# Kernel tuning notes

Hardware: AMD Instinct MI355X
Metric: run time of the kernel (lower is better)

## Reference

```python
import jax, jax.numpy as jnp
import numpy as np

N, F_IN, H, C1, CH, NCLS, E = 10000, 512, 8, 30, 64, 64, 160000


def gat_conv(x, src, dst, W, a_src, a_dst, b):
    # x: [N, Fin]; W: [Fin, H*C]; a_src/a_dst: [H, C]; b: [H*C]
    n, = (x.shape[0],)
    C = a_src.shape[1]
    h = (x @ W).reshape(n, H, C)                        # [N,H,C]
    asrc = jnp.einsum('nhc,hc->nh', h, a_src)           # [N,H]
    adst = jnp.einsum('nhc,hc->nh', h, a_dst)           # [N,H]
    alpha = jax.nn.leaky_relu(asrc[src] + adst[dst], 0.2)  # [E,H]
    # segment softmax over incoming edges of each destination node
    m = jax.ops.segment_max(alpha, dst, num_segments=n)
    m = jax.lax.stop_gradient(jnp.where(jnp.isfinite(m), m, 0.0))
    e = jnp.exp(alpha - m[dst])
    s = jax.ops.segment_sum(e, dst, num_segments=n)
    w = e / (s[dst] + 1e-16)                            # [E,H]
    out = jax.ops.segment_sum(w[:, :, None] * h[src], dst, num_segments=n)
    return out.reshape(n, H * C) + b


def setup_inputs() -> dict:
    key = jax.random.key(0)
    ks = jax.random.split(key, 12)
    x = jax.random.normal(ks[0], (N, F_IN), dtype=jnp.float32)
    edge_index = jax.random.randint(ks[1], (2, E), 0, N, dtype=jnp.int64)
    sc = lambda fin: 1.0 / np.sqrt(fin)
    return {
        'x': x,
        'edge_index': edge_index,
        'W1': jax.random.normal(ks[2], (F_IN, H * C1), jnp.float32) * sc(F_IN),
        'a1_src': jax.random.normal(ks[3], (H, C1), jnp.float32) * sc(C1),
        'a1_dst': jax.random.normal(ks[4], (H, C1), jnp.float32) * sc(C1),
        'b1': jnp.zeros((H * C1,), jnp.float32),
        'W2': jax.random.normal(ks[5], (H * C1, H * CH), jnp.float32) * sc(H * C1),
        'a2_src': jax.random.normal(ks[6], (H, CH), jnp.float32) * sc(CH),
        'a2_dst': jax.random.normal(ks[7], (H, CH), jnp.float32) * sc(CH),
        'b2': jnp.zeros((H * CH,), jnp.float32),
        'Wlin': jax.random.normal(ks[8], (H * CH, NCLS), jnp.float32) * sc(H * CH),
        'blin': jnp.zeros((NCLS,), jnp.float32),
    }


def reference(x, edge_index, W1, a1_src, a1_dst, b1, W2, a2_src, a2_dst, b2, Wlin, blin):
    n = x.shape[0]
    loops = jnp.arange(n, dtype=edge_index.dtype)
    src = jnp.concatenate([edge_index[0], loops])
    dst = jnp.concatenate([edge_index[1], loops])
    # dropout is identity in eval mode
    h1 = jax.nn.elu(gat_conv(x, src, dst, W1, a1_src, a1_dst, b1))
    h = gat_conv(h1, src, dst, W2, a2_src, a2_dst, b2)
    out = h @ Wlin + blin
    return (out, h)
```

## Files before the change

kernel.cpp:

```cpp
#include <hip/hip_runtime.h>
#include <type_traits>

typedef unsigned short ushort_t;
typedef float v4f __attribute__((ext_vector_type(4)));
typedef short v8s __attribute__((ext_vector_type(8)));
typedef unsigned short u16x8 __attribute__((ext_vector_type(8)));
typedef unsigned short u16x4v __attribute__((ext_vector_type(4)));

#define NN    10000
#define NP    10048
#define EE    160000
#define FIN   512
#define NH    8
#define C1    30
#define HC1   240
#define HC1P  256
#define C2    64
#define HC2   512
#define NCLS  64

#define TS1 (HC1P * FIN)
#define TS2 (HC2 * HC1P)
#define TS3 (NCLS * HC2)
#define XS  (NN * FIN / 4)

#define GLOBAL_AS __attribute__((address_space(1)))
#define LDS_AS    __attribute__((address_space(3)))

__device__ __forceinline__ void async_cp16(const void* g, void* l) {
    __builtin_amdgcn_global_load_lds((const GLOBAL_AS unsigned int*)g,
                                     (LDS_AS unsigned int*)l, 16, 0, 0);
}


__global__ __launch_bounds__(1024) void scan_kernel(const int* __restrict__ counts,
                                                    int* __restrict__ row_start,
                                                    int* __restrict__ cursor, int n) {
    __shared__ int sums[1024];
    int t = threadIdx.x;
    const int chunk = (n + 1023) / 1024;
    int beg = t * chunk;
    int end = min(beg + chunk, n);
    int s = 0;
    for (int i = beg; i < end; ++i) s += counts[i];
    sums[t] = s;
    __syncthreads();
    for (int off = 1; off < 1024; off <<= 1) {
        int v = (t >= off) ? sums[t - off] : 0;
        __syncthreads();
        sums[t] += v;
        __syncthreads();
    }
    int run = (t == 0) ? 0 : sums[t - 1];
    for (int i = beg; i < end; ++i) {
        row_start[i] = run;
        cursor[i] = run;
        run += counts[i];
    }
    if (t == 1023) row_start[n] = sums[1023];
}

__global__ __launch_bounds__(256) void scatter_kernel(const int* __restrict__ src,
                                                      const int* __restrict__ dst,
                                                      int* __restrict__ cursor,
                                                      int* __restrict__ edge_src, int E) {
    int e = blockIdx.x * blockDim.x + threadIdx.x;
    if (e < E) {
        int d = dst[e];
        int pos = atomicAdd(&cursor[d], 1);
        edge_src[pos] = src[e];
    }
}


__device__ __forceinline__ void split1(float v, ushort_t& h, ushort_t& l) {
    unsigned u = __float_as_uint(v);
    unsigned rh = u + 0x7FFFu + ((u >> 16) & 1u);
    h = (ushort_t)(rh >> 16);
    float hf = __uint_as_float((unsigned)h << 16);
    float rem = v - hf;
    unsigned u2 = __float_as_uint(rem);
    unsigned rl = u2 + 0x7FFFu + ((u2 >> 16) & 1u);
    l = (ushort_t)(rl >> 16);
}

__device__ __forceinline__ ushort_t f2bf(float v) {
    unsigned u = __float_as_uint(v);
    return (ushort_t)((u + 0x7FFFu + ((u >> 16) & 1u)) >> 16);
}

__device__ __forceinline__ float bf2f(ushort_t u) {
    return __uint_as_float((unsigned)u << 16);
}


__global__ __launch_bounds__(256) void prep_kernel(
    const float* __restrict__ x,
    const float* __restrict__ W1, const float* __restrict__ W2,
    const float* __restrict__ Wl,
    const float* __restrict__ a1s, const float* __restrict__ a1d,
    const int* __restrict__ dst,
    ushort_t* __restrict__ xh, ushort_t* __restrict__ xl,
    ushort_t* __restrict__ t1h, ushort_t* __restrict__ t1l,
    ushort_t* __restrict__ t2h, ushort_t* __restrict__ t2l,
    ushort_t* __restrict__ t3h, ushort_t* __restrict__ t3l,
    float* __restrict__ a1sP, float* __restrict__ a1dP,
    int* __restrict__ counts) {
    int idx = blockIdx.x * 256 + threadIdx.x;
    if (idx < XS) {
        int i = idx << 2;
        float4 v = *(const float4*)(x + i);
        ushort_t h, l;
        u16x4v hh, ll;
        split1(v.x, h, l); hh[0] = h; ll[0] = l;
        split1(v.y, h, l); hh[1] = h; ll[1] = l;
        split1(v.z, h, l); hh[2] = h; ll[2] = l;
        split1(v.w, h, l); hh[3] = h; ll[3] = l;
        *(u16x4v*)(xh + i) = hh;
        *(u16x4v*)(xl + i) = ll;
        return;
    }
    idx -= XS;
    if (idx < TS1) {
        int n = idx >> 9, k = idx & 511;
        int cc = n & 31;
        float v = (cc < 30) ? W1[(size_t)k * HC1 + ((n >> 5) * 30 + cc)] : 0.f;
        ushort_t h, l;
        split1(v, h, l);
        t1h[idx] = h;
        t1l[idx] = l;
    } else if (idx < TS1 + TS2) {
        int lo = idx - TS1;
        int n = lo >> 8, k = lo & 255;
        int cc = k & 31;
        float v = (cc < 30) ? W2[(size_t)((k >> 5) * 30 + cc) * HC2 + n] : 0.f;
        ushort_t h, l;
        split1(v, h, l);
        t2h[lo] = h;
        t2l[lo] = l;
    } else if (idx < TS1 + TS2 + TS3) {
        int lo = idx - TS1 - TS2;
        int n = lo >> 9, k = lo & 511;
        float v = Wl[(size_t)k * NCLS + n];
        ushort_t h, l;
        split1(v, h, l);
        t3h[lo] = h;
        t3l[lo] = l;
    } else if (idx < TS1 + TS2 + TS3 + 2 * HC1P) {
        int j = idx - (TS1 + TS2 + TS3);
        int c = j & (HC1P - 1);
        int cc = c & 31;
        float vs = (cc < 30) ? a1s[(c >> 5) * 30 + cc] : 0.f;
        float vd = (cc < 30) ? a1d[(c >> 5) * 30 + cc] : 0.f;
        if (j < HC1P) a1sP[c] = vs;
        else          a1dP[c] = vd;
    } else {
        int e = idx - (TS1 + TS2 + TS3 + 2 * HC1P);
        if (e < EE) atomicAdd(&counts[dst[e]], 1);
    }
}


template <int TM, int TN, bool BIAS, bool WF32, bool WBF, int TPH>
__global__ __launch_bounds__(256) void gemm_mfma(const ushort_t* __restrict__ Ath,
                                                 const ushort_t* __restrict__ Atl,
                                                 const ushort_t* __restrict__ Bth,
                                                 const ushort_t* __restrict__ Btl,
                                                 const float* __restrict__ bias,
                                                 float* __restrict__ C,
                                                 ushort_t* __restrict__ Cbf,
                                                 const float* __restrict__ att_s,
                                                 const float* __restrict__ att_d,
                                                 float* __restrict__ asrc,
                                                 float* __restrict__ adst,
                                                 int M, int K, int CS) {
    constexpr int ROWS = 32 * TM;
    constexpr int BN   = 32 * TN;
    constexpr int CA = ROWS / 16;
    constexpr int CB = BN / 16;
    constexpr int TOT = 2 * (CA + CB);
    static_assert(TOT % 4 == 0, "chunks must split across 4 waves");
    constexpr int PW = TOT / 4;
    constexpr int AOFF_L = ROWS * 32;
    constexpr int BOFF_H = ROWS * 64;
    constexpr int BOFF_L = ROWS * 64 + BN * 32;
    constexpr int BUFSZ  = (ROWS + BN) * 64;
    __shared__ ushort_t lds[2][BUFSZ];

    const int t    = threadIdx.x;
    const int lane = t & 63;
    const int wave = t >> 6;
    const int quad = lane >> 4;
    const int l16  = lane & 15;
    const int wm   = wave >> 1;
    const int wn   = wave & 1;
    const int bm   = blockIdx.x * ROWS;
    const int bn   = blockIdx.y * BN;

    const ushort_t* gsrc[PW];
    int ldst[PW];
    {
        const int rr = lane >> 2;
        const int q  = lane & 3;
        const int sw = (q ^ (rr & 3)) << 3;
        #pragma unroll
        for (int c = 0; c < PW; ++c) {
            int j = wave * PW + c;
            const ushort_t* gt;
            int off, jj, gb;
            if (j < CA)               { gt = Ath; jj = j;              off = 0;      gb = bm; }
            else if (j < 2 * CA)      { gt = Atl; jj = j - CA;         off = AOFF_L; gb = bm; }
            else if (j < 2 * CA + CB) { gt = Bth; jj = j - 2 * CA;     off = BOFF_H; gb = bn; }
            else                      { gt = Btl; jj = j - 2 * CA - CB; off = BOFF_L; gb = bn; }
            gsrc[c] = gt + (size_t)(gb + jj * 16 + rr) * K + sw;
            ldst[c] = off + jj * 512;
        }
    }

    int aoff[TM], boff[TN];
    #pragma unroll
    for (int tt = 0; tt < TM; ++tt) {
        int r = wm * 16 * TM + tt * 16 + l16;
        aoff[tt] = r * 32 + ((quad ^ (r & 3)) << 3);
    }
    #pragma unroll
    for (int tn = 0; tn < TN; ++tn) {
        int r = wn * 16 * TN + tn * 16 + l16;
        boff[tn] = r * 32 + ((quad ^ (r & 3)) << 3);
    }

    v4f acc[TM][TN];
    #pragma unroll
    for (int i = 0; i < TM; ++i)
        #pragma unroll
        for (int j = 0; j < TN; ++j) acc[i][j] = 0.f;

    #pragma unroll
    for (int c = 0; c < PW; ++c) async_cp16(gsrc[c], &lds[0][ldst[c]]);

    int cur = 0;
    for (int k0 = 0; k0 < K; k0 += 32) {
        __syncthreads();
        if (k0 + 32 < K) {
            #pragma unroll
            for (int c = 0; c < PW; ++c)
                async_cp16(gsrc[c] + k0 + 32, &lds[cur ^ 1][ldst[c]]);
        }
        const ushort_t* bufc = lds[cur];
        v8s ah[TM], al2[TM], bh2[TN], bl2[TN];
        #pragma unroll
        for (int tt = 0; tt < TM; ++tt) {
            ah[tt]  = *(const v8s*)&bufc[aoff[tt]];
            al2[tt] = *(const v8s*)&bufc[AOFF_L + aoff[tt]];
        }
        #pragma unroll
        for (int tn = 0; tn < TN; ++tn) {
            bh2[tn] = *(const v8s*)&bufc[BOFF_H + boff[tn]];
            bl2[tn] = *(const v8s*)&bufc[BOFF_L + boff[tn]];
        }
        #pragma unroll
        for (int tm = 0; tm < TM; ++tm)
            #pragma unroll
            for (int tn = 0; tn < TN; ++tn) {
                acc[tm][tn] = __builtin_amdgcn_mfma_f32_16x16x32_bf16(
                    ah[tm], bh2[tn], acc[tm][tn], 0, 0, 0);
                acc[tm][tn] = __builtin_amdgcn_mfma_f32_16x16x32_bf16(
                    ah[tm], bl2[tn], acc[tm][tn], 0, 0, 0);
                acc[tm][tn] = __builtin_amdgcn_mfma_f32_16x16x32_bf16(
                    al2[tm], bh2[tn], acc[tm][tn], 0, 0, 0);
            }
        cur ^= 1;
    }

    #pragma unroll
    for (int tm = 0; tm < TM; ++tm) {
        #pragma unroll
        for (int tn = 0; tn < TN; ++tn) {
            int row0 = bm + wm * 16 * TM + tm * 16 + quad * 4;
            int col  = bn + wn * 16 * TN + tn * 16 + l16;
            float badd = BIAS ? bias[col] : 0.f;
            #pragma unroll
            for (int reg = 0; reg < 4; ++reg) {
                int row = row0 + reg;
                if (row < M) {
                    float v = acc[tm][tn][reg] + badd;
                    if (WF32) C[(size_t)row * CS + col] = v;
                    if (WBF) Cbf[(size_t)row * CS + col] = f2bf(v);
                }
            }
        }
    }

    if constexpr (TPH > 0) {
        constexpr int GR = TN / TPH;
        float aS[TN], aD[TN];
        #pragma unroll
        for (int tn = 0; tn < TN; ++tn) {
            int col = bn + wn * 16 * TN + tn * 16 + l16;
            aS[tn] = att_s[col];
            aD[tn] = att_d[col];
        }
        #pragma unroll
        for (int tm = 0; tm < TM; ++tm) {
            #pragma unroll
            for (int reg = 0; reg < 4; ++reg) {
                #pragma unroll
                for (int g = 0; g < GR; ++g) {
                    float ss = 0.f, sd = 0.f;
                    #pragma unroll
                    for (int ti = 0; ti < TPH; ++ti) {
                        int tn = g * TPH + ti;
                        ss += acc[tm][tn][reg] * aS[tn];
                        sd += acc[tm][tn][reg] * aD[tn];
                    }
                    #pragma unroll
                    for (int off = 1; off < 16; off <<= 1) {
                        ss += __shfl_xor(ss, off);
                        sd += __shfl_xor(sd, off);
                    }
                    if (l16 == 0) {
                        int row = bm + wm * 16 * TM + tm * 16 + quad * 4 + reg;
                        if (row < M) {
                            int head = (bn + wn * 16 * TN + g * 16 * TPH) / (16 * TPH);
                            asrc[row * NH + head] = ss;
                            adst[row * NH + head] = sd;
                        }
                    }
                }
            }
        }
    }
}


template <int CPL, bool ELU, bool OSPLIT, bool OF32, bool PADB>
__global__ __launch_bounds__(256) void agg_u(const ushort_t* __restrict__ hb,
                                             const float* __restrict__ asrc,
                                             const float* __restrict__ adst,
                                             const int* __restrict__ row_start,
                                             const int* __restrict__ edge_src,
                                             const float* __restrict__ bias,
                                             float* __restrict__ outf,
                                             ushort_t* __restrict__ outh,
                                             ushort_t* __restrict__ outl,
                                             int n) {
    constexpr int RSB = CPL * 64;
    using VT = typename std::conditional<CPL == 8, u16x8, u16x4v>::type;
    const int d    = (blockIdx.x * blockDim.x + threadIdx.x) >> 6;
    const int lane = threadIdx.x & 63;
    if (d >= n) return;
    const int head = lane >> 3;

    const float adh = (lane < NH) ? adst[d * NH + lane] : 0.f;

    float m, s;
    float ac[CPL];
    {
        float a = (lane < NH) ? asrc[d * NH + lane] + adh : 0.f;
        a = fmaxf(a, 0.2f * a);
        m = a;
        s = 1.f;
        VT u = *(const VT*)(hb + (size_t)d * RSB + CPL * lane);
        #pragma unroll
        for (int i = 0; i < CPL; ++i) ac[i] = bf2f(u[i]);
    }

    const int beg = row_start[d];
    const int end = row_start[d + 1];

    auto LD = [&](int eb, VT* rr, float* ss) {
        int i0 = edge_src[eb], i1 = edge_src[eb + 1];
        int i2 = edge_src[eb + 2], i3 = edge_src[eb + 3];
        rr[0] = *(const VT*)(hb + (size_t)i0 * RSB + CPL * lane);
        rr[1] = *(const VT*)(hb + (size_t)i1 * RSB + CPL * lane);
        rr[2] = *(const VT*)(hb + (size_t)i2 * RSB + CPL * lane);
        rr[3] = *(const VT*)(hb + (size_t)i3 * RSB + CPL * lane);
        if (lane < NH) {
            ss[0] = asrc[i0 * NH + lane];
            ss[1] = asrc[i1 * NH + lane];
            ss[2] = asrc[i2 * NH + lane];
            ss[3] = asrc[i3 * NH + lane];
        } else {
            ss[0] = ss[1] = ss[2] = ss[3] = 0.f;
        }
    };
    auto PR = [&](const VT* rr, const float* ss) {
        float a0 = ss[0] + adh, a1 = ss[1] + adh, a2 = ss[2] + adh, a3 = ss[3] + adh;
        a0 = fmaxf(a0, 0.2f * a0);
        a1 = fmaxf(a1, 0.2f * a1);
        a2 = fmaxf(a2, 0.2f * a2);
        a3 = fmaxf(a3, 0.2f * a3);
        float mn = fmaxf(m, fmaxf(fmaxf(a0, a1), fmaxf(a2, a3)));
        float al = __expf(m - mn);
        float w0 = __expf(a0 - mn);
        float w1 = __expf(a1 - mn);
        float w2 = __expf(a2 - mn);
        float w3 = __expf(a3 - mn);
        s = s * al + (w0 + w1) + (w2 + w3);
        m = mn;
        float alc = __shfl(al, head);
        float c0 = __shfl(w0, head);
        float c1 = __shfl(w1, head);
        float c2 = __shfl(w2, head);
        float c3 = __shfl(w3, head);
        #pragma unroll
        for (int i = 0; i < CPL; ++i)
            ac[i] = ac[i] * alc + c0 * bf2f(rr[0][i]) + c1 * bf2f(rr[1][i]) +
                    c2 * bf2f(rr[2][i]) + c3 * bf2f(rr[3][i]);
    };

    int e = beg;
    const int ng = (end - beg) >> 2;
    if (ng > 0) {
        VT cr[4];
        float cs[4];
        LD(e, cr, cs);
        for (int g = 1; g < ng; ++g) {
            VT nr[4];
            float ns[4];
            LD(e + 4 * g, nr, ns);
            PR(cr, cs);
            #pragma unroll
            for (int j = 0; j < 4; ++j) { cr[j] = nr[j]; cs[j] = ns[j]; }
        }
        PR(cr, cs);
        e += 4 * ng;
    }
    for (; e < end; ++e) {
        int i0 = edge_src[e];
        VT r0 = *(const VT*)(hb + (size_t)i0 * RSB + CPL * lane);
        float a0 = (lane < NH) ? asrc[i0 * NH + lane] + adh : 0.f;
        a0 = fmaxf(a0, 0.2f * a0);
        float mn = fmaxf(m, a0);
        float al = __expf(m - mn);
        float w0 = __expf(a0 - mn);
        s = s * al + w0;
        m = mn;
        float alc = __shfl(al, head);
        float c0w = __shfl(w0, head);
        #pragma unroll
        for (int i = 0; i < CPL; ++i) ac[i] = ac[i] * alc + c0w * bf2f(r0[i]);
    }

    float inv = 1.f / s;
    float ivc = __shfl(inv, head);
    float o[CPL];
    if constexpr (PADB) {
        const int c = CPL * lane;
        const int cc = c & 31;
        const int bbase = (c >> 5) * 30 + cc;
        #pragma unroll
        for (int i = 0; i < CPL; ++i) {
            float b = (cc + i < 30) ? bias[bbase + i] : 0.f;
            o[i] = ac[i] * ivc + b;
        }
    } else {
        #pragma unroll
        for (int i = 0; i < CPL; ++i) o[i] = ac[i] * ivc + bias[CPL * lane + i];
    }
    if (ELU) {
        #pragma unroll
        for (int i = 0; i < CPL; ++i) o[i] = (o[i] > 0.f) ? o[i] : __expf(o[i]) - 1.f;
    }
    if constexpr (OSPLIT) {
        VT hh, ll;
        #pragma unroll
        for (int i = 0; i < CPL; ++i) {
            ushort_t h2, l2;
            split1(o[i], h2, l2);
            hh[i] = h2;
            ll[i] = l2;
        }
        *(VT*)(outh + (size_t)d * RSB + CPL * lane) = hh;
        *(VT*)(outl + (size_t)d * RSB + CPL * lane) = ll;
    }
    if constexpr (OF32) {
        float4* orow = (float4*)(outf + (size_t)d * RSB);
        #pragma unroll
        for (int q = 0; q < CPL / 4; ++q) {
            float4 v;
            v.x = o[4 * q + 0];
            v.y = o[4 * q + 1];
            v.z = o[4 * q + 2];
            v.w = o[4 * q + 3];
            orow[(CPL / 4) * lane + q] = v;
        }
    }
}


extern "C" void kernel_launch(void* const* d_in, const int* in_sizes, int n_in,
                              void* d_out, int out_size, void* d_ws, size_t ws_size,
                              hipStream_t stream) {
    const float* x      = (const float*)d_in[0];
    const int*   eidx   = (const int*)d_in[1];
    const float* W1     = (const float*)d_in[2];
    const float* a1_src = (const float*)d_in[3];
    const float* a1_dst = (const float*)d_in[4];
    const float* b1     = (const float*)d_in[5];
    const float* W2     = (const float*)d_in[6];
    const float* a2_src = (const float*)d_in[7];
    const float* a2_dst = (const float*)d_in[8];
    const float* b2     = (const float*)d_in[9];
    const float* Wlin   = (const float*)d_in[10];
    const float* blin   = (const float*)d_in[11];

    const int* src = eidx;
    const int* dst = eidx + EE;

    float* out0  = (float*)d_out;
    float* h_out = (float*)d_out + (size_t)NN * NCLS;

    float* f = (float*)d_ws;
    float* asrc1 = f;
    float* adst1 = asrc1 + NN * NH;
    float* asrc2 = adst1 + NN * NH;
    float* adst2 = asrc2 + NN * NH;
    float* a1sP  = adst2 + NN * NH;
    float* a1dP  = a1sP + HC1P;
    ushort_t* xh    = (ushort_t*)(a1dP + HC1P);
    ushort_t* xl    = xh + (size_t)NP * FIN;
    ushort_t* w1t_h = xl + (size_t)NP * FIN;
    ushort_t* w1t_l = w1t_h + TS1;
    ushort_t* w2t_h = w1t_l + TS1;
    ushort_t* w2t_l = w2t_h + TS2;
    ushort_t* wlt_h = w2t_l + TS2;
    ushort_t* wlt_l = wlt_h + TS3;
    ushort_t* h1p_bf = wlt_l + TS3;
    ushort_t* h1h    = h1p_bf + (size_t)NN * HC1P;
    ushort_t* h1l    = h1h + (size_t)NP * HC1P;
    ushort_t* h2p_bf = h1l + (size_t)NP * HC1P;
    ushort_t* h2h    = h2p_bf + (size_t)NN * HC2;
    ushort_t* h2l    = h2h + (size_t)NP * HC2;
    int* counts    = (int*)(h2l + (size_t)NP * HC2);
    int* cursor    = counts + NN;
    int* row_start = cursor + NN;
    int* edge_src  = row_start + NN + 1;

    hipMemsetAsync(counts, 0, NN * sizeof(int), stream);

    {
        const int total = XS + TS1 + TS2 + TS3 + 2 * HC1P + EE;
        prep_kernel<<<(total + 255) / 256, 256, 0, stream>>>(
            x, W1, W2, Wlin, a1_src, a1_dst, dst, xh, xl, w1t_h, w1t_l,
            w2t_h, w2t_l, wlt_h, wlt_l, a1sP, a1dP, counts);
    }
    scan_kernel<<<1, 1024, 0, stream>>>(counts, row_start, cursor, NN);
    scatter_kernel<<<(EE + 255) / 256, 256, 0, stream>>>(src, dst, cursor,
                                                         edge_src, EE);

    const int MB = (NN + 63) / 64;

    {
        dim3 grid(MB, HC1P / 128);
        gemm_mfma<2, 4, false, false, true, 2><<<grid, 256, 0, stream>>>(
            xh, xl, w1t_h, w1t_l, nullptr, nullptr, h1p_bf,
            a1sP, a1dP, asrc1, adst1, NN, FIN, HC1P);
    }
    agg_u<4, true, true, false, true><<<(NN + 3) / 4, 256, 0, stream>>>(
        h1p_bf, asrc1, adst1, row_start, edge_src, b1, nullptr, h1h, h1l, NN);

    {
        dim3 grid(MB, HC2 / 128);
        gemm_mfma<2, 4, false, false, true, 4><<<grid, 256, 0, stream>>>(
            h1h, h1l, w2t_h, w2t_l, nullptr, nullptr, h2p_bf,
            a2_src, a2_dst, asrc2, adst2, NN, HC1P, HC2);
    }
    agg_u<8, false, true, true, false><<<(NN + 3) / 4, 256, 0, stream>>>(
        h2p_bf, asrc2, adst2, row_start, edge_src, b2, h_out, h2h, h2l, NN);

    {
        dim3 grid((NN + 31) / 32, NCLS / 64);
        gemm_mfma<1, 2, true, true, false, 0><<<grid, 256, 0, stream>>>(
            h2h, h2l, wlt_h, wlt_l, blin, out0, nullptr,
            nullptr, nullptr, nullptr, nullptr, NN, HC2, NCLS);
    }
}
```

Before: 223.6 us.

## Load GEMM B operand directly to registers with triple-buffered A in LDS

The split-bf16 MFMA GEMM now stages only the A tile through LDS, using three buffers with async global-to-LDS copies issued two k-steps ahead. The B operand is loaded straight from global memory into registers, one step ahead with double buffering. A single __syncthreads is replaced by explicit vmcnt waits plus a barrier, which cuts LDS traffic and synchronisation per k-step. The scan kernel also moves from a 1024-wide LDS Hillis-Steele scan to wave shuffles. Risks: B loads are no longer shared across waves, the hand-counted vmcnt values must match the number of loads actually in flight, and the loop assumes NS is even.

```diff
diff --git a/kernel.cpp b/kernel.cpp
--- a/kernel.cpp
+++ b/kernel.cpp
@@ -32,32 +32,53 @@
                                      (LDS_AS unsigned int*)l, 16, 0, 0);
 }
 
+template <int N>
+__device__ __forceinline__ void wait_vmcnt() {
+    if constexpr (N == 0)       asm volatile("s_waitcnt vmcnt(0)" ::: "memory");
+    else if constexpr (N == 4)  asm volatile("s_waitcnt vmcnt(4)" ::: "memory");
+    else if constexpr (N == 5)  asm volatile("s_waitcnt vmcnt(5)" ::: "memory");
+    else if constexpr (N == 8)  asm volatile("s_waitcnt vmcnt(8)" ::: "memory");
+    else if constexpr (N == 10) asm volatile("s_waitcnt vmcnt(10)" ::: "memory");
+    else static_assert(N == 0, "unsupported vmcnt literal");
+}
+
 
 __global__ __launch_bounds__(1024) void scan_kernel(const int* __restrict__ counts,
                                                     int* __restrict__ row_start,
                                                     int* __restrict__ cursor, int n) {
-    __shared__ int sums[1024];
+    __shared__ int wsum[16];
     int t = threadIdx.x;
     const int chunk = (n + 1023) / 1024;
     int beg = t * chunk;
     int end = min(beg + chunk, n);
     int s = 0;
     for (int i = beg; i < end; ++i) s += counts[i];
-    sums[t] = s;
+    const int lane = t & 63, w = t >> 6;
+    int v = s;
+    #pragma unroll
+    for (int off = 1; off < 64; off <<= 1) {
+        int u = __shfl_up(v, off);
+        if (lane >= off) v += u;
+    }
+    if (lane == 63) wsum[w] = v;
     __syncthreads();
-    for (int off = 1; off < 1024; off <<= 1) {
-        int v = (t >= off) ? sums[t - off] : 0;
-        __syncthreads();
-        sums[t] += v;
-        __syncthreads();
-    }
-    int run = (t == 0) ? 0 : sums[t - 1];
+    if (w == 0) {
+        int ws = (lane < 16) ? wsum[lane] : 0;
+        #pragma unroll
+        for (int off = 1; off < 16; off <<= 1) {
+            int u = __shfl_up(ws, off);
+            if (lane >= off) ws += u;
+        }
+        if (lane < 16) wsum[lane] = ws;
+    }
+    __syncthreads();
+    int run = (w ? wsum[w - 1] : 0) + v - s;
     for (int i = beg; i < end; ++i) {
         row_start[i] = run;
         cursor[i] = run;
         run += counts[i];
     }
-    if (t == 1023) row_start[n] = sums[1023];
+    if (t == 1023) row_start[n] = run;
 }
 
 __global__ __launch_bounds__(256) void scatter_kernel(const int* __restrict__ src,
@@ -176,16 +197,8 @@
                                                  int M, int K, int CS) {
     constexpr int ROWS = 32 * TM;
     constexpr int BN   = 32 * TN;
-    constexpr int CA = ROWS / 16;
-    constexpr int CB = BN / 16;
-    constexpr int TOT = 2 * (CA + CB);
-    static_assert(TOT % 4 == 0, "chunks must split across 4 waves");
-    constexpr int PW = TOT / 4;
-    constexpr int AOFF_L = ROWS * 32;
-    constexpr int BOFF_H = ROWS * 64;
-    constexpr int BOFF_L = ROWS * 64 + BN * 32;
-    constexpr int BUFSZ  = (ROWS + BN) * 64;
-    __shared__ ushort_t lds[2][BUFSZ];
+    constexpr int ASZ  = ROWS * 64;
+    __shared__ ushort_t lds[3 * ASZ];
 
     const int t    = threadIdx.x;
     const int lane = t & 63;
@@ -197,36 +210,34 @@
     const int bm   = blockIdx.x * ROWS;
     const int bn   = blockIdx.y * BN;
 
-    const ushort_t* gsrc[PW];
-    int ldst[PW];
+    const ushort_t* gsrcA[TM];
+    int ldstA[TM];
     {
         const int rr = lane >> 2;
         const int q  = lane & 3;
         const int sw = (q ^ (rr & 3)) << 3;
         #pragma unroll
-        for (int c = 0; c < PW; ++c) {
-            int j = wave * PW + c;
-            const ushort_t* gt;
-            int off, jj, gb;
-            if (j < CA)               { gt = Ath; jj = j;              off = 0;      gb = bm; }
-            else if (j < 2 * CA)      { gt = Atl; jj = j - CA;         off = AOFF_L; gb = bm; }
-            else if (j < 2 * CA + CB) { gt = Bth; jj = j - 2 * CA;     off = BOFF_H; gb = bn; }
-            else                      { gt = Btl; jj = j - 2 * CA - CB; off = BOFF_L; gb = bn; }
-            gsrc[c] = gt + (size_t)(gb + jj * 16 + rr) * K + sw;
-            ldst[c] = off + jj * 512;
-        }
-    }
-
-    int aoff[TM], boff[TN];
+        for (int c = 0; c < TM; ++c) {
+            int jA = wave * TM + c;
+            const ushort_t* gt = (jA < 2 * TM) ? Ath : Atl;
+            int jj = jA & (2 * TM - 1);
+            gsrcA[c] = gt + (size_t)(bm + jj * 16 + rr) * K + sw;
+            ldstA[c] = ((jA < 2 * TM) ? 0 : ROWS * 32) + jj * 512;
+        }
+    }
+    int aoffH[TM];
     #pragma unroll
     for (int tt = 0; tt < TM; ++tt) {
         int r = wm * 16 * TM + tt * 16 + l16;
-        aoff[tt] = r * 32 + ((quad ^ (r & 3)) << 3);
-    }
+        aoffH[tt] = r * 32 + ((quad ^ (r & 3)) << 3);
+    }
+    const ushort_t* bp_h[TN];
+    const ushort_t* bp_l[TN];
     #pragma unroll
     for (int tn = 0; tn < TN; ++tn) {
-        int r = wn * 16 * TN + tn * 16 + l16;
-        boff[tn] = r * 32 + ((quad ^ (r & 3)) << 3);
+        size_t ro = (size_t)(bn + wn * 16 * TN + tn * 16 + l16) * K + quad * 8;
+        bp_h[tn] = Bth + ro;
+        bp_l[tn] = Btl + ro;
     }
 
     v4f acc[TM][TN];
@@ -235,41 +246,62 @@
         #pragma unroll
         for (int j = 0; j < TN; ++j) acc[i][j] = 0.f;
 
-    #pragma unroll
-    for (int c = 0; c < PW; ++c) async_cp16(gsrc[c], &lds[0][ldst[c]]);
-
-    int cur = 0;
-    for (int k0 = 0; k0 < K; k0 += 32) {
-        __syncthreads();
-        if (k0 + 32 < K) {
+    const int NS = K >> 5;
+
+    #pragma unroll
+    for (int c = 0; c < TM; ++c) async_cp16(gsrcA[c], &lds[ldstA[c]]);
+    v8s B0h[TN], B0l[TN], B1h[TN], B1l[TN];
+    #pragma unroll
+    for (int tn = 0; tn < TN; ++tn) {
+        B0h[tn] = *(const v8s*)(bp_h[tn]);
+        B0l[tn] = *(const v8s*)(bp_l[tn]);
+    }
+    #pragma unroll
+    for (int c = 0; c < TM; ++c) async_cp16(gsrcA[c] + 32, &lds[ASZ + ldstA[c]]);
+
+    auto body = [&](int j, v8s (&cbh)[TN], v8s (&cbl)[TN],
+                    v8s (&nbh)[TN], v8s (&nbl)[TN]) {
+        if (j + 1 < NS) wait_vmcnt<2 * TN + TM>();
+        else            wait_vmcnt<2 * TN>();
+        __builtin_amdgcn_s_barrier();
+        asm volatile("" ::: "memory");
+        if (j + 1 < NS) {
+            const int kk = (j + 1) << 5;
             #pragma unroll
-            for (int c = 0; c < PW; ++c)
-                async_cp16(gsrc[c] + k0 + 32, &lds[cur ^ 1][ldst[c]]);
-        }
-        const ushort_t* bufc = lds[cur];
-        v8s ah[TM], al2[TM], bh2[TN], bl2[TN];
+            for (int tn = 0; tn < TN; ++tn) {
+                nbh[tn] = *(const v8s*)(bp_h[tn] + kk);
+                nbl[tn] = *(const v8s*)(bp_l[tn] + kk);
+            }
+        }
+        if (j + 2 < NS) {
+            const int kk = (j + 2) << 5;
+            const int ab = (j + 2) % 3;
+            #pragma unroll
+            for (int c = 0; c < TM; ++c)
+                async_cp16(gsrcA[c] + kk, &lds[ab * ASZ + ldstA[c]]);
+        }
+        const ushort_t* Ab = &lds[(j % 3) * ASZ];
+        v8s ah[TM], al2[TM];
         #pragma unroll
         for (int tt = 0; tt < TM; ++tt) {
-            ah[tt]  = *(const v8s*)&bufc[aoff[tt]];
-            al2[tt] = *(const v8s*)&bufc[AOFF_L + aoff[tt]];
-        }
-        #pragma unroll
-        for (int tn = 0; tn < TN; ++tn) {
-            bh2[tn] = *(const v8s*)&bufc[BOFF_H + boff[tn]];
-            bl2[tn] = *(const v8s*)&bufc[BOFF_L + boff[tn]];
+            ah[tt]  = *(const v8s*)&Ab[aoffH[tt]];
+            al2[tt] = *(const v8s*)&Ab[ROWS * 32 + aoffH[tt]];
         }
         #pragma unroll
         for (int tm = 0; tm < TM; ++tm)
             #pragma unroll
             for (int tn = 0; tn < TN; ++tn) {
                 acc[tm][tn] = __builtin_amdgcn_mfma_f32_16x16x32_bf16(
-                    ah[tm], bh2[tn], acc[tm][tn], 0, 0, 0);
+                    ah[tm], cbh[tn], acc[tm][tn], 0, 0, 0);
                 acc[tm][tn] = __builtin_amdgcn_mfma_f32_16x16x32_bf16(
-                    ah[tm], bl2[tn], acc[tm][tn], 0, 0, 0);
+                    ah[tm], cbl[tn], acc[tm][tn], 0, 0, 0);
                 acc[tm][tn] = __builtin_amdgcn_mfma_f32_16x16x32_bf16(
-                    al2[tm], bh2[tn], acc[tm][tn], 0, 0, 0);
+                    al2[tm], cbh[tn], acc[tm][tn], 0, 0, 0);
             }
-        cur ^= 1;
+    };
+    for (int j = 0; j < NS; j += 2) {
+        body(j, B0h, B0l, B1h, B1l);
+        body(j + 1, B1h, B1l, B0h, B0l);
     }
 
     #pragma unroll
```

Result: slower. 264.4 us (+18.2%).

## Fuse CSR count, scan and scatter into one persistent kernel with grid barriers

Applied to the files above, without the earlier changes.

Replaces the memset, the edge counting inside prep_kernel, the single-block scan kernel and the scatter kernel with one 256-block persistent kernel. Its phases are separated by atomic-counter grid barriers, and the scan uses wave shuffles. The intent is to remove several launches and the slow serial 1024-thread scan. In exchange it relies on all 256 blocks being co-resident for the spin barriers, which is not guaranteed in general, and on the barrier counters being reset by prep_kernel before each call.

```diff
diff --git a/kernel.cpp b/kernel.cpp
--- a/kernel.cpp
+++ b/kernel.cpp
@@ -24,52 +24,14 @@
 #define TS3 (NCLS * HC2)
 #define XS  (NN * FIN / 4)
 
+#define CSRB 256
+
 #define GLOBAL_AS __attribute__((address_space(1)))
 #define LDS_AS    __attribute__((address_space(3)))
 
 __device__ __forceinline__ void async_cp16(const void* g, void* l) {
     __builtin_amdgcn_global_load_lds((const GLOBAL_AS unsigned int*)g,
                                      (LDS_AS unsigned int*)l, 16, 0, 0);
-}
-
-
-__global__ __launch_bounds__(1024) void scan_kernel(const int* __restrict__ counts,
-                                                    int* __restrict__ row_start,
-                                                    int* __restrict__ cursor, int n) {
-    __shared__ int sums[1024];
-    int t = threadIdx.x;
-    const int chunk = (n + 1023) / 1024;
-    int beg = t * chunk;
-    int end = min(beg + chunk, n);
-    int s = 0;
-    for (int i = beg; i < end; ++i) s += counts[i];
-    sums[t] = s;
-    __syncthreads();
-    for (int off = 1; off < 1024; off <<= 1) {
-        int v = (t >= off) ? sums[t - off] : 0;
-        __syncthreads();
-        sums[t] += v;
-        __syncthreads();
-    }
-    int run = (t == 0) ? 0 : sums[t - 1];
-    for (int i = beg; i < end; ++i) {
-        row_start[i] = run;
-        cursor[i] = run;
-        run += counts[i];
-    }
-    if (t == 1023) row_start[n] = sums[1023];
-}
-
-__global__ __launch_bounds__(256) void scatter_kernel(const int* __restrict__ src,
-                                                      const int* __restrict__ dst,
-                                                      int* __restrict__ cursor,
-                                                      int* __restrict__ edge_src, int E) {
-    int e = blockIdx.x * blockDim.x + threadIdx.x;
-    if (e < E) {
-        int d = dst[e];
-        int pos = atomicAdd(&cursor[d], 1);
-        edge_src[pos] = src[e];
-    }
 }
 
 
@@ -99,13 +61,13 @@
     const float* __restrict__ W1, const float* __restrict__ W2,
     const float* __restrict__ Wl,
     const float* __restrict__ a1s, const float* __restrict__ a1d,
-    const int* __restrict__ dst,
     ushort_t* __restrict__ xh, ushort_t* __restrict__ xl,
     ushort_t* __restrict__ t1h, ushort_t* __restrict__ t1l,
     ushort_t* __restrict__ t2h, ushort_t* __restrict__ t2l,
     ushort_t* __restrict__ t3h, ushort_t* __restrict__ t3l,
     float* __restrict__ a1sP, float* __restrict__ a1dP,
-    int* __restrict__ counts) {
+    int* __restrict__ bars) {
+    if (blockIdx.x == 0 && threadIdx.x < 4) bars[threadIdx.x] = 0;
     int idx = blockIdx.x * 256 + threadIdx.x;
     if (idx < XS) {
         int i = idx << 2;
@@ -154,9 +116,68 @@
         float vd = (cc < 30) ? a1d[(c >> 5) * 30 + cc] : 0.f;
         if (j < HC1P) a1sP[c] = vs;
         else          a1dP[c] = vd;
-    } else {
-        int e = idx - (TS1 + TS2 + TS3 + 2 * HC1P);
-        if (e < EE) atomicAdd(&counts[dst[e]], 1);
+    }
+}
+
+
+__device__ __forceinline__ void gbar(int* bar) {
+    __syncthreads();
+    if (threadIdx.x == 0) {
+        __threadfence();
+        atomicAdd(bar, 1);
+        while (atomicAdd(bar, 0) < CSRB) __builtin_amdgcn_s_sleep(8);
+        __threadfence();
+    }
+    __syncthreads();
+}
+
+__global__ __launch_bounds__(256) void csr_kernel(const int* __restrict__ src,
+                                                  const int* __restrict__ dst,
+                                                  int* __restrict__ counts,
+                                                  int* __restrict__ row_start,
+                                                  int* __restrict__ cursor,
+                                                  int* __restrict__ edge_src,
+                                                  int* __restrict__ bars) {
+    const int t = threadIdx.x;
+    const int gtid = blockIdx.x * 256 + t;
+    const int gsz = CSRB * 256;
+    for (int i = gtid; i < NN; i += gsz) counts[i] = 0;
+    gbar(bars + 0);
+    for (int e = gtid; e < EE; e += gsz) atomicAdd(&counts[dst[e]], 1);
+    gbar(bars + 1);
+    if (blockIdx.x == 0) {
+        __shared__ int ws[4];
+        const volatile int* vc = (const volatile int*)counts;
+        int lc[40];
+        int beg = t * 40;
+        int nel = min(beg + 40, NN) - beg;
+        if (nel < 0) nel = 0;
+        int s = 0;
+        for (int i = 0; i < nel; ++i) { lc[i] = vc[beg + i]; s += lc[i]; }
+        const int lane = t & 63, w = t >> 6;
+        int v = s;
+        #pragma unroll
+        for (int off = 1; off < 64; off <<= 1) {
+            int u = __shfl_up(v, off);
+            if (lane >= off) v += u;
+        }
+        if (lane == 63) ws[w] = v;
+        __syncthreads();
+        int woff = 0;
+        for (int i = 0; i < w; ++i) woff += ws[i];
+        int run = woff + v - s;
+        for (int i = 0; i < nel; ++i) {
+            row_start[beg + i] = run;
+            cursor[beg + i] = run;
+            run += lc[i];
+        }
+        if (t == 255) row_start[NN] = run;
+    }
+    gbar(bars + 2);
+    for (int e = gtid; e < EE; e += gsz) {
+        int d = dst[e];
+        int pos = atomicAdd(&cursor[d], 1);
+        edge_src[pos] = src[e];
     }
 }
 
@@ -536,18 +557,16 @@
     int* cursor    = counts + NN;
     int* row_start = cursor + NN;
     int* edge_src  = row_start + NN + 1;
-
-    hipMemsetAsync(counts, 0, NN * sizeof(int), stream);
+    int* bars      = edge_src + EE;
 
     {
-        const int total = XS + TS1 + TS2 + TS3 + 2 * HC1P + EE;
+        const int total = XS + TS1 + TS2 + TS3 + 2 * HC1P;
         prep_kernel<<<(total + 255) / 256, 256, 0, stream>>>(
-            x, W1, W2, Wlin, a1_src, a1_dst, dst, xh, xl, w1t_h, w1t_l,
-            w2t_h, w2t_l, wlt_h, wlt_l, a1sP, a1dP, counts);
-    }
-    scan_kernel<<<1, 1024, 0, stream>>>(counts, row_start, cursor, NN);
-    scatter_kernel<<<(EE + 255) / 256, 256, 0, stream>>>(src, dst, cursor,
-                                                         edge_src, EE);
+            x, W1, W2, Wlin, a1_src, a1_dst, xh, xl, w1t_h, w1t_l,
+            w2t_h, w2t_l, wlt_h, wlt_l, a1sP, a1dP, bars);
+    }
+    csr_kernel<<<CSRB, 256, 0, stream>>>(src, dst, counts, row_start, cursor,
+                                         edge_src, bars);
 
     const int MB = (NN + 63) / 64;
 
```

Result: slower. 285.4 us (+27.7%).
